# Kernel optimization log

Hardware: AMD Instinct MI355X
Metric: run time of the kernel (lower is better)

## Reference

```python
import jax, jax.numpy as jnp
import numpy as np

C_OUT = 16
C_IN = 16
L0 = 64        # layer_sizes[0]
H = 128        # hidden width
D_IN = C_IN * L0  # 1024, flattened per-point input dim


def _uniform(key, shape, fan_in):
    bound = 1.0 / np.sqrt(fan_in)
    return jax.random.uniform(key, shape, jnp.float32, -bound, bound)


def setup_inputs() -> dict:
    key = jax.random.key(0)
    ks = jax.random.split(key, 7)
    x = jax.random.normal(ks[0], (65536, C_IN, L0), jnp.float32)
    # Stacked per-output-channel MLP weights (torch Linear transposed: [in, out])
    W1 = _uniform(ks[1], (C_OUT, D_IN, H), D_IN)
    b1 = _uniform(ks[2], (C_OUT, H), D_IN)
    W2 = _uniform(ks[3], (C_OUT, H, H), H)
    b2 = _uniform(ks[4], (C_OUT, H, H)[:2], H)
    W3 = _uniform(ks[5], (C_OUT, H, 1), H)
    b3 = _uniform(ks[6], (C_OUT, 1), H)
    return {"x": x, "W1": W1, "b1": b1, "W2": W2, "b2": b2, "W3": W3, "b3": b3}


def reference(x, W1, b1, W2, b2, W3, b3):
    # x: [N, C_in, L0] -> flatten per point to [N, D_IN]
    N = x.shape[0]
    xf = x.reshape(N, -1)
    # Batched per-output-channel GEMMs (replaces Python loop over channels_out)
    h = jax.nn.relu(jnp.einsum('nd,cdh->cnh', xf, W1) + b1[:, None, :])   # [C, N, H]
    h = jax.nn.relu(jnp.einsum('cnh,chk->cnk', h, W2) + b2[:, None, :])   # [C, N, H]
    out = jnp.einsum('cnh,cho->cno', h, W3) + b3[:, None, :]              # [C, N, 1]
    # squeeze(-1) then permute channel axis to the end: [N, C_out]
    return out[..., 0].T
```

## Files before the change

### kernel.cpp

```cpp
#include <hip/hip_runtime.h>
#include <cstdint>

typedef unsigned short u16;
typedef __attribute__((ext_vector_type(4))) float f32x4;
typedef __attribute__((ext_vector_type(8))) __bf16 bf16x8;
typedef __attribute__((ext_vector_type(8))) u16 u16x8;

#define C_OUT 16
#define D_IN 1024
#define HDIM 128
#define NPTS 65536
#define BN 128
#define BK 64

__device__ __forceinline__ u16 f2bf(float f){
  uint32_t u = __builtin_bit_cast(uint32_t, f);
  u += 0x7FFFu + ((u >> 16) & 1u);
  return (u16)(u >> 16);
}

__device__ __forceinline__ void gload_lds16(const void* g, void* l){
  __builtin_amdgcn_global_load_lds((const __attribute__((address_space(1))) void*)g,
                                   (__attribute__((address_space(3))) void*)l, 16, 0, 0);
}

__global__ __launch_bounds__(256) void transpose_cvt(const float* __restrict__ src,
                                                     u16* __restrict__ dst, int R, int C){
  __shared__ float tile[32][33];
  int ch = blockIdx.z;
  int r0 = blockIdx.y * 32, c0 = blockIdx.x * 32;
  const float* s = src + (size_t)ch * R * C;
  u16* d = dst + (size_t)ch * R * C;
  int tx = threadIdx.x, ty = threadIdx.y;
  for (int i = ty; i < 32; i += 8) tile[i][tx] = s[(size_t)(r0 + i) * C + c0 + tx];
  __syncthreads();
  for (int i = ty; i < 32; i += 8) d[(size_t)(c0 + i) * R + r0 + tx] = f2bf(tile[tx][i]);
}

__global__ __launch_bounds__(256) void cvt_x_kernel(const float4* __restrict__ src,
                                                    u16x8* __restrict__ dst, int n8){
  int stride = gridDim.x * 256;
  for (int i = blockIdx.x * 256 + threadIdx.x; i < n8; i += stride){
    float4 v0 = src[2 * i];
    float4 v1 = src[2 * i + 1];
    u16x8 o = { f2bf(v0.x), f2bf(v0.y), f2bf(v0.z), f2bf(v0.w),
                f2bf(v1.x), f2bf(v1.y), f2bf(v1.z), f2bf(v1.w) };
    dst[i] = o;
  }
}

__global__ __launch_bounds__(256, 3) void mlp_fused(const u16* __restrict__ xb,
    const u16* __restrict__ W1T, const u16* __restrict__ W2T,
    const float* __restrict__ b1, const float* __restrict__ b2,
    const float* __restrict__ W3, const float* __restrict__ b3,
    float* __restrict__ out){
  __shared__ __align__(16) u16 smem[2 * BN * BK];
  __shared__ float outb[BN];
  u16* As = smem;
  u16* Bs = smem + BN * BK;

  const int t = threadIdx.x;
  const int wave = t >> 6, lane = t & 63;
  const int q = lane >> 4, s = lane & 15;
  const int wr = (wave >> 1) * 64, wc = (wave & 1) * 64;

  const int p = blockIdx.x;
  const int o = p >> 3;
  const int c = o & 15;
  const int T = ((o >> 4) << 3) | (p & 7);
  const int n0 = T * BN;

  const u16* w1c = W1T + (size_t)c * HDIM * D_IN;

  f32x4 acc[4][4];
#pragma unroll
  for (int i = 0; i < 4; i++)
#pragma unroll
    for (int j = 0; j < 4; j++) acc[i][j] = (f32x4){0.f, 0.f, 0.f, 0.f};

  for (int kt = 0; kt < D_IN / BK; kt++){
#pragma unroll
    for (int ii = 0; ii < 4; ii++){
      int hbase = wave * 32 + ii * 8;
      int h = hbase + (lane >> 3);
      int k = kt * BK + (((lane & 7) ^ (h & 7)) * 8);
      gload_lds16(w1c + (size_t)h * D_IN + k, &Bs[hbase * BK]);
    }
#pragma unroll
    for (int ii = 0; ii < 4; ii++){
      int rbase = wave * 32 + ii * 8;
      int row = rbase + (lane >> 3);
      int k = kt * BK + (((lane & 7) ^ (row & 7)) * 8);
      gload_lds16(xb + (size_t)(n0 + row) * D_IN + k, &As[rbase * BK]);
    }
    __syncthreads();
#pragma unroll
    for (int ks = 0; ks < 2; ks++){
      bf16x8 a[4], b[4];
#pragma unroll
      for (int i = 0; i < 4; i++){
        int m = wr + i * 16 + s;
        int ch = ks * 4 + q;
        a[i] = __builtin_bit_cast(bf16x8, *(const u16x8*)&As[m * BK + ((ch ^ (m & 7)) * 8)]);
      }
#pragma unroll
      for (int j = 0; j < 4; j++){
        int hh = wc + j * 16 + s;
        int ch = ks * 4 + q;
        b[j] = __builtin_bit_cast(bf16x8, *(const u16x8*)&Bs[hh * BK + ((ch ^ (hh & 7)) * 8)]);
      }
#pragma unroll
      for (int i = 0; i < 4; i++)
#pragma unroll
        for (int j = 0; j < 4; j++)
          acc[i][j] = __builtin_amdgcn_mfma_f32_16x16x32_bf16(a[i], b[j], acc[i][j], 0, 0, 0);
    }
    __syncthreads();
  }

  float b1v[4];
#pragma unroll
  for (int j = 0; j < 4; j++) b1v[j] = b1[c * HDIM + wc + j * 16 + s];
  u16* h1s = smem;
#pragma unroll
  for (int i = 0; i < 4; i++)
#pragma unroll
    for (int j = 0; j < 4; j++)
#pragma unroll
      for (int r = 0; r < 4; r++){
        float v = fmaxf(acc[i][j][r] + b1v[j], 0.f);
        int m = wr + i * 16 + q * 4 + r;
        int h = wc + j * 16 + s;
        h1s[m * HDIM + (((h >> 3) ^ (m & 7)) * 8) + (h & 7)] = f2bf(v);
      }
  __syncthreads();

  const u16* w2c = W2T + (size_t)c * HDIM * HDIM;
  f32x4 acc2[4][4];
#pragma unroll
  for (int i = 0; i < 4; i++)
#pragma unroll
    for (int j = 0; j < 4; j++) acc2[i][j] = (f32x4){0.f, 0.f, 0.f, 0.f};
#pragma unroll
  for (int ks = 0; ks < 4; ks++){
    bf16x8 a[4], b[4];
#pragma unroll
    for (int i = 0; i < 4; i++){
      int m = wr + i * 16 + s;
      int ch = ks * 4 + q;
      a[i] = __builtin_bit_cast(bf16x8, *(const u16x8*)&h1s[m * HDIM + ((ch ^ (m & 7)) * 8)]);
    }
#pragma unroll
    for (int j = 0; j < 4; j++){
      int col = wc + j * 16 + s;
      b[j] = __builtin_bit_cast(bf16x8, *(const u16x8*)(w2c + (size_t)col * HDIM + ks * 32 + q * 8));
    }
#pragma unroll
    for (int i = 0; i < 4; i++)
#pragma unroll
      for (int j = 0; j < 4; j++)
        acc2[i][j] = __builtin_amdgcn_mfma_f32_16x16x32_bf16(a[i], b[j], acc2[i][j], 0, 0, 0);
  }

  float b2v[4], w3v[4];
#pragma unroll
  for (int j = 0; j < 4; j++){
    b2v[j] = b2[c * HDIM + wc + j * 16 + s];
    w3v[j] = W3[c * HDIM + wc + j * 16 + s];
  }
  float part[4][4];
#pragma unroll
  for (int i = 0; i < 4; i++)
#pragma unroll
    for (int r = 0; r < 4; r++) part[i][r] = 0.f;
#pragma unroll
  for (int i = 0; i < 4; i++)
#pragma unroll
    for (int j = 0; j < 4; j++)
#pragma unroll
      for (int r = 0; r < 4; r++){
        float hv = fmaxf(acc2[i][j][r] + b2v[j], 0.f);
        part[i][r] = fmaf(hv, w3v[j], part[i][r]);
      }
#pragma unroll
  for (int mask = 1; mask <= 8; mask <<= 1)
#pragma unroll
    for (int i = 0; i < 4; i++)
#pragma unroll
      for (int r = 0; r < 4; r++) part[i][r] += __shfl_xor(part[i][r], mask, 64);

  if (s == 0 && wc == 0){
#pragma unroll
    for (int i = 0; i < 4; i++)
#pragma unroll
      for (int r = 0; r < 4; r++) outb[wr + i * 16 + q * 4 + r] = part[i][r];
  }
  __syncthreads();
  if (s == 0 && wc == 64){
#pragma unroll
    for (int i = 0; i < 4; i++)
#pragma unroll
      for (int r = 0; r < 4; r++) outb[wr + i * 16 + q * 4 + r] += part[i][r];
  }
  __syncthreads();
  if (t < BN) out[(size_t)(n0 + t) * C_OUT + c] = outb[t] + b3[c];
}

__global__ __launch_bounds__(256) void mlp_naive(const float* __restrict__ x,
    const float* __restrict__ W1, const float* __restrict__ b1,
    const float* __restrict__ W2, const float* __restrict__ b2,
    const float* __restrict__ W3, const float* __restrict__ b3,
    float* __restrict__ out){
  __shared__ float xs[16 * D_IN];
  __shared__ float h1[16 * HDIM];
  __shared__ float h2[16 * HDIM];
  int c = blockIdx.x & 15;
  int n0 = (blockIdx.x >> 4) * 16;
  int t = threadIdx.x;
  for (int i = t; i < 16 * D_IN; i += 256) xs[i] = x[(size_t)n0 * D_IN + i];
  __syncthreads();
  int h = t & 127, ng = t >> 7;
  const float* w1c = W1 + (size_t)c * D_IN * HDIM;
  float a1[8];
#pragma unroll
  for (int nn = 0; nn < 8; nn++) a1[nn] = 0.f;
  for (int d = 0; d < D_IN; d++){
    float w = w1c[(size_t)d * HDIM + h];
#pragma unroll
    for (int nn = 0; nn < 8; nn++) a1[nn] = fmaf(xs[(ng * 8 + nn) * D_IN + d], w, a1[nn]);
  }
  float bb = b1[c * HDIM + h];
#pragma unroll
  for (int nn = 0; nn < 8; nn++) h1[(ng * 8 + nn) * HDIM + h] = fmaxf(a1[nn] + bb, 0.f);
  __syncthreads();
  const float* w2c = W2 + (size_t)c * HDIM * HDIM;
  float a2[8];
#pragma unroll
  for (int nn = 0; nn < 8; nn++) a2[nn] = 0.f;
  for (int k = 0; k < HDIM; k++){
    float w = w2c[(size_t)k * HDIM + h];
#pragma unroll
    for (int nn = 0; nn < 8; nn++) a2[nn] = fmaf(h1[(ng * 8 + nn) * HDIM + k], w, a2[nn]);
  }
  bb = b2[c * HDIM + h];
#pragma unroll
  for (int nn = 0; nn < 8; nn++) h2[(ng * 8 + nn) * HDIM + h] = fmaxf(a2[nn] + bb, 0.f);
  __syncthreads();
  if (t < 16){
    float ssum = 0.f;
    for (int hh = 0; hh < HDIM; hh++) ssum = fmaf(h2[t * HDIM + hh], W3[c * HDIM + hh], ssum);
    out[(size_t)(n0 + t) * C_OUT + c] = ssum + b3[c];
  }
}

extern "C" void kernel_launch(void* const* d_in, const int* in_sizes, int n_in,
                              void* d_out, int out_size, void* d_ws, size_t ws_size,
                              hipStream_t stream){
  const float* x  = (const float*)d_in[0];
  const float* W1 = (const float*)d_in[1];
  const float* b1 = (const float*)d_in[2];
  const float* W2 = (const float*)d_in[3];
  const float* b2 = (const float*)d_in[4];
  const float* W3 = (const float*)d_in[5];
  const float* b3 = (const float*)d_in[6];
  float* out = (float*)d_out;

  const size_t W1T_elems = (size_t)C_OUT * HDIM * D_IN;
  const size_t W2T_elems = (size_t)C_OUT * HDIM * HDIM;
  const size_t xb_elems  = (size_t)NPTS * D_IN;
  const size_t ws_bytes  = (W1T_elems + W2T_elems + xb_elems) * 2;

  if (ws_size < ws_bytes){
    mlp_naive<<<(NPTS / 16) * C_OUT, 256, 0, stream>>>(x, W1, b1, W2, b2, W3, b3, out);
    return;
  }

  u16* W1T = (u16*)d_ws;
  u16* W2T = W1T + W1T_elems;
  u16* xb  = W2T + W2T_elems;
  transpose_cvt<<<dim3(HDIM / 32, D_IN / 32, C_OUT), dim3(32, 8), 0, stream>>>(W1, W1T, D_IN, HDIM);
  transpose_cvt<<<dim3(HDIM / 32, HDIM / 32, C_OUT), dim3(32, 8), 0, stream>>>(W2, W2T, HDIM, HDIM);
  cvt_x_kernel<<<8192, 256, 0, stream>>>((const float4*)x, (u16x8*)xb, (int)(xb_elems / 8));

  const int grid = (NPTS / BN) * C_OUT;
  mlp_fused<<<grid, 256, 0, stream>>>(xb, W1T, W2T, b1, b2, W3, b3, out);
}
```

Before: 695.3 us.

## Load GEMM1 operands directly from global into registers with double buffering

Replaces the LDS-staged first GEMM (global_load_lds into swizzled shared tiles with two barriers per K step) with direct per-lane vector loads from global into MFMA operand registers, software-pipelined across two register sets. This removes LDS traffic and __syncthreads from the main loop and shrinks shared memory to the h1 buffer. In exchange, each wave re-reads A and B fragments from global/L2 with no cross-wave sharing, which raises global traffic and register pressure.

```diff
diff --git a/kernel.cpp b/kernel.cpp
--- a/kernel.cpp
+++ b/kernel.cpp
@@ -11,17 +11,11 @@
 #define HDIM 128
 #define NPTS 65536
 #define BN 128
-#define BK 64
 
 __device__ __forceinline__ u16 f2bf(float f){
   uint32_t u = __builtin_bit_cast(uint32_t, f);
   u += 0x7FFFu + ((u >> 16) & 1u);
   return (u16)(u >> 16);
-}
-
-__device__ __forceinline__ void gload_lds16(const void* g, void* l){
-  __builtin_amdgcn_global_load_lds((const __attribute__((address_space(1))) void*)g,
-                                   (__attribute__((address_space(3))) void*)l, 16, 0, 0);
 }
 
 __global__ __launch_bounds__(256) void transpose_cvt(const float* __restrict__ src,
@@ -54,10 +48,8 @@
     const float* __restrict__ b1, const float* __restrict__ b2,
     const float* __restrict__ W3, const float* __restrict__ b3,
     float* __restrict__ out){
-  __shared__ __align__(16) u16 smem[2 * BN * BK];
+  __shared__ __align__(16) u16 smem[BN * HDIM];
   __shared__ float outb[BN];
-  u16* As = smem;
-  u16* Bs = smem + BN * BK;
 
   const int t = threadIdx.x;
   const int wave = t >> 6, lane = t & 63;
@@ -70,7 +62,11 @@
   const int T = ((o >> 4) << 3) | (p & 7);
   const int n0 = T * BN;
 
-  const u16* w1c = W1T + (size_t)c * HDIM * D_IN;
+  int aoff[4], boff[4];
+#pragma unroll
+  for (int i = 0; i < 4; i++) aoff[i] = (n0 + wr + i * 16 + s) * D_IN + q * 8;
+#pragma unroll
+  for (int j = 0; j < 4; j++) boff[j] = (c * HDIM + wc + j * 16 + s) * D_IN + q * 8;
 
   f32x4 acc[4][4];
 #pragma unroll
@@ -78,44 +74,29 @@
 #pragma unroll
     for (int j = 0; j < 4; j++) acc[i][j] = (f32x4){0.f, 0.f, 0.f, 0.f};
 
-  for (int kt = 0; kt < D_IN / BK; kt++){
-#pragma unroll
-    for (int ii = 0; ii < 4; ii++){
-      int hbase = wave * 32 + ii * 8;
-      int h = hbase + (lane >> 3);
-      int k = kt * BK + (((lane & 7) ^ (h & 7)) * 8);
-      gload_lds16(w1c + (size_t)h * D_IN + k, &Bs[hbase * BK]);
-    }
-#pragma unroll
-    for (int ii = 0; ii < 4; ii++){
-      int rbase = wave * 32 + ii * 8;
-      int row = rbase + (lane >> 3);
-      int k = kt * BK + (((lane & 7) ^ (row & 7)) * 8);
-      gload_lds16(xb + (size_t)(n0 + row) * D_IN + k, &As[rbase * BK]);
-    }
-    __syncthreads();
-#pragma unroll
-    for (int ks = 0; ks < 2; ks++){
-      bf16x8 a[4], b[4];
-#pragma unroll
-      for (int i = 0; i < 4; i++){
-        int m = wr + i * 16 + s;
-        int ch = ks * 4 + q;
-        a[i] = __builtin_bit_cast(bf16x8, *(const u16x8*)&As[m * BK + ((ch ^ (m & 7)) * 8)]);
-      }
-#pragma unroll
-      for (int j = 0; j < 4; j++){
-        int hh = wc + j * 16 + s;
-        int ch = ks * 4 + q;
-        b[j] = __builtin_bit_cast(bf16x8, *(const u16x8*)&Bs[hh * BK + ((ch ^ (hh & 7)) * 8)]);
-      }
-#pragma unroll
-      for (int i = 0; i < 4; i++)
-#pragma unroll
-        for (int j = 0; j < 4; j++)
-          acc[i][j] = __builtin_amdgcn_mfma_f32_16x16x32_bf16(a[i], b[j], acc[i][j], 0, 0, 0);
-    }
-    __syncthreads();
+  auto loadset = [&](int kk, u16x8* A, u16x8* B){
+#pragma unroll
+    for (int i = 0; i < 4; i++) A[i] = *(const u16x8*)(xb + aoff[i] + kk * 32);
+#pragma unroll
+    for (int j = 0; j < 4; j++) B[j] = *(const u16x8*)(W1T + boff[j] + kk * 32);
+  };
+  auto mfmaset = [&](u16x8* A, u16x8* B){
+#pragma unroll
+    for (int i = 0; i < 4; i++)
+#pragma unroll
+      for (int j = 0; j < 4; j++)
+        acc[i][j] = __builtin_amdgcn_mfma_f32_16x16x32_bf16(
+            __builtin_bit_cast(bf16x8, A[i]), __builtin_bit_cast(bf16x8, B[j]),
+            acc[i][j], 0, 0, 0);
+  };
+
+  u16x8 av0[4], bv0[4], av1[4], bv1[4];
+  loadset(0, av0, bv0);
+  for (int kk = 0; kk < 32; kk += 2){
+    loadset(kk + 1, av1, bv1);
+    mfmaset(av0, bv0);
+    if (kk + 2 < 32) loadset(kk + 2, av0, bv0);
+    mfmaset(av1, bv1);
   }
 
   float b1v[4];
```

Measured after the change: 1.355 ms. +94.9%, slower.
